# Performance work log

Hardware: AMD Instinct MI355X
Metric: run time of the kernel (lower is better)

Reference implementation:

```python
import jax, jax.numpy as jnp
import numpy as np

BN_EPS = 1e-5
DIST_EPS = 1e-8


def setup_inputs() -> dict:
    key = jax.random.key(0)
    ks = jax.random.split(key, 8)
    B, N, S, D1, D2 = 8, 16384, 2048, 128, 256
    return {
        "xyz1": jax.random.normal(ks[0], (B, N, 3), jnp.float32),
        "xyz2": jax.random.normal(ks[1], (B, S, 3), jnp.float32),
        "points1": jax.random.normal(ks[2], (B, N, D1), jnp.float32),
        "points2": jax.random.normal(ks[3], (B, S, D2), jnp.float32),
        "w1": jax.random.normal(ks[4], (256, 384), jnp.float32) * 0.05,
        "b1": jnp.zeros((256,), jnp.float32),
        "g1": jnp.ones((256,), jnp.float32),
        "be1": jnp.zeros((256,), jnp.float32),
        "w2": jax.random.normal(ks[5], (128, 256), jnp.float32) * 0.05,
        "b2": jnp.zeros((128,), jnp.float32),
        "g2": jnp.ones((128,), jnp.float32),
        "be2": jnp.zeros((128,), jnp.float32),
        "fa1": jax.random.normal(ks[6], (16, 128), jnp.float32) * 0.1,
        "fa2": jax.random.normal(ks[7], (128, 16), jnp.float32) * 0.1,
    }


def _three_interp(xyz1, xyz2, points2):
    # squared pairwise distance [B,N,S]
    d = (jnp.sum(xyz1 ** 2, -1)[:, :, None]
         + jnp.sum(xyz2 ** 2, -1)[:, None, :]
         - 2.0 * jnp.einsum("bnc,bsc->bns", xyz1, xyz2))
    neg_d, idx = jax.lax.top_k(-d, 3)          # 3 smallest distances
    dist = -neg_d                               # [B,N,3]
    recip = 1.0 / (dist + DIST_EPS)
    w = recip / jnp.sum(recip, -1, keepdims=True)
    B, N, _ = idx.shape
    D = points2.shape[-1]
    gathered = jnp.take_along_axis(
        points2, idx.reshape(B, N * 3)[..., None], axis=1
    ).reshape(B, N, 3, D)
    return jnp.sum(gathered * w[..., None], axis=-2)  # [B,N,D]


def _bn_relu(h, g, be):
    # train-mode BatchNorm1d: stats over (batch, length)
    mu = jnp.mean(h, axis=(0, 1))
    var = jnp.var(h, axis=(0, 1))
    return jax.nn.relu(g * (h - mu) / jnp.sqrt(var + BN_EPS) + be)


def reference(xyz1, xyz2, points1, points2, w1, b1, g1, be1,
              w2, b2, g2, be2, fa1, fa2):
    interp = _three_interp(xyz1, xyz2, points2)          # [B,N,256]
    x = jnp.concatenate([points1, interp], axis=-1)      # [B,N,384]
    # 1x1 Conv1d + BN + ReLU stack (channel-last)
    x = _bn_relu(jnp.einsum("bnc,oc->bno", x, w1) + b1, g1, be1)  # [B,N,256]
    x = _bn_relu(jnp.einsum("bnc,oc->bno", x, w2) + b2, g2, be2)  # [B,N,128]
    # channel attention (SE-style, avg + max pool over length)
    def fc(v):  # v: [B,C]
        return jax.nn.relu(v @ fa1.T) @ fa2.T
    avg = jnp.mean(x, axis=1)
    mx = jnp.max(x, axis=1)
    scale = jax.nn.sigmoid(fc(avg) + fc(mx))             # [B,C]
    return x * scale[:, None, :]                          # [B,N,128]
```

## Files before the change

### kernel.cpp

```cpp
#include <hip/hip_runtime.h>
#include <math.h>

constexpr int BB = 8;
constexpr int NN = 16384;
constexpr int SS = 2048;
constexpr int D2 = 256;
constexpr int H1 = 256;
constexpr int H2 = 128;
constexpr int MM = BB * NN;
constexpr int LDB = 40;

typedef __attribute__((ext_vector_type(8))) short short8;
typedef __attribute__((ext_vector_type(16))) float f32x16;

__device__ __forceinline__ unsigned short f2b(float f) {
    union { float f; unsigned u; } v; v.f = f;
    unsigned r = v.u + 0x7FFFu + ((v.u >> 16) & 1u);
    return (unsigned short)(r >> 16);
}
__device__ __forceinline__ unsigned pk2(float lo, float hi) {
    return (unsigned)f2b(lo) | ((unsigned)f2b(hi) << 16);
}
__device__ __forceinline__ float b2f_lo(unsigned p) { return __uint_as_float(p << 16); }
__device__ __forceinline__ float b2f_hi(unsigned p) { return __uint_as_float(p & 0xFFFF0000u); }

__global__ void k_init(float* __restrict__ st1, float* __restrict__ st2,
                       float* __restrict__ psum, int* __restrict__ pmax) {
    int t = threadIdx.x;
    if (t < 512) st1[t] = 0.f;
    if (t < 256) st2[t] = 0.f;
    if (t < 1024) { psum[t] = 0.f; pmax[t] = 0; }
}

__global__ void k_wprep(const float* __restrict__ w1, const float* __restrict__ w2,
                        unsigned short* __restrict__ w1b, unsigned short* __restrict__ w2b) {
    int i = blockIdx.x * 256 + threadIdx.x;
    if (i < H1 * 384) w1b[i] = f2b(w1[i]);
    if (i < H2 * 256) w2b[i] = f2b(w2[i]);
}

__global__ __launch_bounds__(256) void k_knn(const float* __restrict__ xyz1,
                                             const float* __restrict__ xyz2,
                                             int* __restrict__ idx,
                                             float* __restrict__ wgt) {
    __shared__ float sx[SS], sy[SS], sz[SS];
    __shared__ unsigned cand[64][20];
    const int b = blockIdx.y;
    const int tid = threadIdx.x;
    const int ql = tid & 63;
    const int chunk = tid >> 6;
    const int n = blockIdx.x * 64 + ql;

    const float* xz2 = xyz2 + (size_t)b * SS * 3;
    for (int s = tid; s < SS; s += 256) {
        sx[s] = xz2[s * 3 + 0];
        sy[s] = xz2[s * 3 + 1];
        sz[s] = xz2[s * 3 + 2];
    }
    __syncthreads();

    const float* q = xyz1 + ((size_t)b * NN + n) * 3;
    const float qx = q[0], qy = q[1], qz = q[2];

    unsigned k0 = 0xFFFFFFFFu, k1 = 0xFFFFFFFFu, k2 = 0xFFFFFFFFu,
             k3 = 0xFFFFFFFFu, k4 = 0xFFFFFFFFu;
    const int s0 = chunk * 512;
#pragma unroll 4
    for (int j = 0; j < 512; ++j) {
        const int s = s0 + j;
        const float dx = qx - sx[s];
        const float dy = qy - sy[s];
        const float dz = qz - sz[s];
        const float d = fmaf(dx, dx, fmaf(dy, dy, dz * dz));
        const unsigned key = (__float_as_uint(d) & 0xFFFFFE00u) | (unsigned)j;
        const bool c0 = key < k0, c1 = key < k1, c2 = key < k2,
                   c3 = key < k3, c4 = key < k4;
        k4 = c4 ? (c3 ? k3 : key) : k4;
        k3 = c3 ? (c2 ? k2 : key) : k3;
        k2 = c2 ? (c1 ? k1 : key) : k2;
        k1 = c1 ? (c0 ? k0 : key) : k1;
        k0 = c0 ? key : k0;
    }
    unsigned* cq = cand[ql] + chunk * 5;
    cq[0] = k0; cq[1] = k1; cq[2] = k2; cq[3] = k3; cq[4] = k4;
    __syncthreads();

    if (tid < 64) {
        const double qxd = (double)qx, qyd = (double)qy, qzd = (double)qz;
        double t0 = 1e300, t1 = 1e300, t2 = 1e300;
        int i0 = 0, i1 = 0, i2 = 0;
#pragma unroll
        for (int ch = 0; ch < 4; ++ch) {
#pragma unroll
            for (int t = 0; t < 5; ++t) {
                const int s = ch * 512 + (int)(cand[tid][ch * 5 + t] & 0x1FFu);
                const double dx = qxd - (double)sx[s];
                const double dy = qyd - (double)sy[s];
                const double dz = qzd - (double)sz[s];
                const double d = fma(dx, dx, fma(dy, dy, dz * dz));
                if (d < t2) {
                    if (d < t0)      { t2 = t1; i2 = i1; t1 = t0; i1 = i0; t0 = d; i0 = s; }
                    else if (d < t1) { t2 = t1; i2 = i1; t1 = d; i1 = s; }
                    else             { t2 = d; i2 = s; }
                }
            }
        }
        const double r0 = 1.0 / (t0 + 1e-8);
        const double r1 = 1.0 / (t1 + 1e-8);
        const double r2 = 1.0 / (t2 + 1e-8);
        const double inv = 1.0 / (r0 + r1 + r2);
        const size_t o = ((size_t)b * NN + n) * 3;
        idx[o + 0] = i0; idx[o + 1] = i1; idx[o + 2] = i2;
        wgt[o + 0] = (float)(r0 * inv);
        wgt[o + 1] = (float)(r1 * inv);
        wgt[o + 2] = (float)(r2 * inv);
    }
}

__global__ __launch_bounds__(256, 2) void k_gemm1(const float* __restrict__ p1,
                                                  const float* __restrict__ p2,
                                                  const int* __restrict__ idx,
                                                  const float* __restrict__ wgt,
                                                  const unsigned short* __restrict__ w1b,
                                                  const float* __restrict__ b1p,
                                                  unsigned short* __restrict__ h1b,
                                                  float* __restrict__ st1) {
    __shared__ __align__(16) unsigned short As[128 * LDB];
    __shared__ __align__(16) unsigned short Bs[256 * LDB];
    __shared__ float sSum[256], sSq[256];

    const int tid = threadIdx.x;
    const int row0 = blockIdx.x * 128;
    const int b = row0 >> 14;
    const float* p2b = p2 + (size_t)b * (SS * D2);

    sSum[tid] = 0.f; sSq[tid] = 0.f;

    const int wave = tid >> 6, lane = tid & 63;
    const int ln = lane & 31, hk = lane >> 5;
    const int wm = (wave & 1) << 6;
    const int wn = (wave >> 1) << 7;
    const int r = tid >> 1, half = tid & 1;

    const size_t o3 = (size_t)(row0 + r) * 3;
    const int j0 = idx[o3], j1 = idx[o3 + 1], j2 = idx[o3 + 2];
    const float wa = wgt[o3], wb = wgt[o3 + 1], wc = wgt[o3 + 2];
    const float* g0 = p2b + ((size_t)j0 << 8);
    const float* g1 = p2b + ((size_t)j1 << 8);
    const float* g2 = p2b + ((size_t)j2 << 8);

    f32x16 acc[2][4];
#pragma unroll
    for (int mt = 0; mt < 2; ++mt)
#pragma unroll
        for (int nt = 0; nt < 4; ++nt)
#pragma unroll
            for (int e = 0; e < 16; ++e) acc[mt][nt][e] = 0.f;

    float4 ra[12];
    uint4 rb[4];

    auto prefetch = [&](int kc) {
        const unsigned short* bsrc = w1b + (size_t)tid * 384 + kc * 32;
        rb[0] = *(const uint4*)(bsrc);
        rb[1] = *(const uint4*)(bsrc + 8);
        rb[2] = *(const uint4*)(bsrc + 16);
        rb[3] = *(const uint4*)(bsrc + 24);
        if (kc < 4) {
            const float* src = p1 + (((size_t)(row0 + r)) << 7) + kc * 32 + half * 16;
            ra[0] = *(const float4*)(src);
            ra[1] = *(const float4*)(src + 4);
            ra[2] = *(const float4*)(src + 8);
            ra[3] = *(const float4*)(src + 12);
        } else {
            const int c2 = kc * 32 - 128 + half * 16;
#pragma unroll
            for (int g = 0; g < 4; ++g) {
                ra[g]     = *(const float4*)(g0 + c2 + g * 4);
                ra[4 + g] = *(const float4*)(g1 + c2 + g * 4);
                ra[8 + g] = *(const float4*)(g2 + c2 + g * 4);
            }
        }
    };

    prefetch(0);

    for (int kc = 0; kc < 12; ++kc) {
        uint4 pa0, pa1;
        if (kc < 4) {
            pa0 = make_uint4(pk2(ra[0].x, ra[0].y), pk2(ra[0].z, ra[0].w),
                             pk2(ra[1].x, ra[1].y), pk2(ra[1].z, ra[1].w));
            pa1 = make_uint4(pk2(ra[2].x, ra[2].y), pk2(ra[2].z, ra[2].w),
                             pk2(ra[3].x, ra[3].y), pk2(ra[3].z, ra[3].w));
        } else {
            float v[16];
#pragma unroll
            for (int g = 0; g < 4; ++g) {
                v[g * 4 + 0] = fmaf(wa, ra[g].x, fmaf(wb, ra[4 + g].x, wc * ra[8 + g].x));
                v[g * 4 + 1] = fmaf(wa, ra[g].y, fmaf(wb, ra[4 + g].y, wc * ra[8 + g].y));
                v[g * 4 + 2] = fmaf(wa, ra[g].z, fmaf(wb, ra[4 + g].z, wc * ra[8 + g].z));
                v[g * 4 + 3] = fmaf(wa, ra[g].w, fmaf(wb, ra[4 + g].w, wc * ra[8 + g].w));
            }
            pa0 = make_uint4(pk2(v[0], v[1]), pk2(v[2], v[3]), pk2(v[4], v[5]), pk2(v[6], v[7]));
            pa1 = make_uint4(pk2(v[8], v[9]), pk2(v[10], v[11]), pk2(v[12], v[13]), pk2(v[14], v[15]));
        }
        const uint4 wb0 = rb[0], wb1 = rb[1], wb2 = rb[2], wb3 = rb[3];

        __syncthreads();
        *(uint4*)&As[r * LDB + half * 16] = pa0;
        *(uint4*)&As[r * LDB + half * 16 + 8] = pa1;
        *(uint4*)&Bs[tid * LDB + 0]  = wb0;
        *(uint4*)&Bs[tid * LDB + 8]  = wb1;
        *(uint4*)&Bs[tid * LDB + 16] = wb2;
        *(uint4*)&Bs[tid * LDB + 24] = wb3;
        __syncthreads();

        if (kc < 11) prefetch(kc + 1);

        short8 af[2][2], bfv[4][2];
#pragma unroll
        for (int mt = 0; mt < 2; ++mt)
#pragma unroll
            for (int ks = 0; ks < 2; ++ks)
                af[mt][ks] = *(const short8*)&As[(wm + mt * 32 + ln) * LDB + ks * 16 + hk * 8];
#pragma unroll
        for (int nt = 0; nt < 4; ++nt)
#pragma unroll
            for (int ks = 0; ks < 2; ++ks)
                bfv[nt][ks] = *(const short8*)&Bs[(wn + nt * 32 + ln) * LDB + ks * 16 + hk * 8];
#pragma unroll
        for (int mt = 0; mt < 2; ++mt)
#pragma unroll
            for (int nt = 0; nt < 4; ++nt)
#pragma unroll
                for (int ks = 0; ks < 2; ++ks)
                    acc[mt][nt] = __builtin_amdgcn_mfma_f32_32x32x16_bf16(
                        af[mt][ks], bfv[nt][ks], acc[mt][nt], 0, 0, 0);
    }

#pragma unroll
    for (int nt = 0; nt < 4; ++nt) {
        const int col = wn + nt * 32 + ln;
        const float bias = b1p[col];
        float ps = 0.f, pq = 0.f;
#pragma unroll
        for (int mt = 0; mt < 2; ++mt) {
#pragma unroll
            for (int e = 0; e < 16; ++e) {
                const int rl = wm + mt * 32 + (e & 3) + ((e >> 2) << 3) + (hk << 2);
                const float o = acc[mt][nt][e] + bias;
                ps += o;
                pq = fmaf(o, o, pq);
                h1b[(((size_t)(row0 + rl)) << 8) + col] = f2b(o);
            }
        }
        atomicAdd(&sSum[col], ps);
        atomicAdd(&sSq[col], pq);
    }
    __syncthreads();
    atomicAdd(&st1[tid], sSum[tid]);
    atomicAdd(&st1[256 + tid], sSq[tid]);
}

__global__ void k_bnprep(const float* __restrict__ st, const float* __restrict__ g,
                         const float* __restrict__ be, float* __restrict__ bn,
                         int C, float invM) {
    int c = blockIdx.x * blockDim.x + threadIdx.x;
    if (c < C) {
        float mean = st[c] * invM;
        float var = st[C + c] * invM - mean * mean;
        float a = g[c] / sqrtf(var + 1e-5f);
        bn[c] = a;
        bn[C + c] = fmaf(-mean, a, be[c]);
    }
}

__global__ __launch_bounds__(256) void k_gemm2(const unsigned short* __restrict__ h1b,
                                               const unsigned short* __restrict__ w2b,
                                               const float* __restrict__ b2p,
                                               const float* __restrict__ bn1,
                                               unsigned short* __restrict__ h2b,
                                               float* __restrict__ st2) {
    __shared__ __align__(16) unsigned short As[128 * LDB];
    __shared__ __align__(16) unsigned short Bs[128 * LDB];
    __shared__ float sBNa[256], sBNb[256];
    __shared__ float sSum[128], sSq[128];

    const int tid = threadIdx.x;
    const int row0 = blockIdx.x * 128;

    sBNa[tid] = bn1[tid];
    sBNb[tid] = bn1[256 + tid];
    if (tid < 128) { sSum[tid] = 0.f; sSq[tid] = 0.f; }

    const int wave = tid >> 6, lane = tid & 63;
    const int ln = lane & 31, hk = lane >> 5;
    const int wm = (wave & 1) << 6, wn = (wave >> 1) << 6;
    const int r = tid >> 1, half = tid & 1;

    f32x16 acc[2][2];
#pragma unroll
    for (int mt = 0; mt < 2; ++mt)
#pragma unroll
        for (int nt = 0; nt < 2; ++nt)
#pragma unroll
            for (int e = 0; e < 16; ++e) acc[mt][nt][e] = 0.f;

    uint4 rA0, rA1, rB0, rB1;
    auto prefetch = [&](int kc) {
        const unsigned short* asrc = h1b + (size_t)(row0 + r) * 256 + kc * 32 + half * 16;
        rA0 = *(const uint4*)asrc;
        rA1 = *(const uint4*)(asrc + 8);
        const unsigned short* bsrc = w2b + (size_t)r * 256 + kc * 32 + half * 16;
        rB0 = *(const uint4*)bsrc;
        rB1 = *(const uint4*)(bsrc + 8);
    };

    prefetch(0);
    __syncthreads();

    for (int kc = 0; kc < 8; ++kc) {
        const int k0 = kc * 32 + half * 16;
        unsigned pw[8] = {rA0.x, rA0.y, rA0.z, rA0.w, rA1.x, rA1.y, rA1.z, rA1.w};
        unsigned po[8];
#pragma unroll
        for (int gi = 0; gi < 8; ++gi) {
            float lo = b2f_lo(pw[gi]);
            float hi = b2f_hi(pw[gi]);
            lo = fmaxf(fmaf(sBNa[k0 + 2 * gi], lo, sBNb[k0 + 2 * gi]), 0.f);
            hi = fmaxf(fmaf(sBNa[k0 + 2 * gi + 1], hi, sBNb[k0 + 2 * gi + 1]), 0.f);
            po[gi] = pk2(lo, hi);
        }
        const uint4 pa0 = make_uint4(po[0], po[1], po[2], po[3]);
        const uint4 pa1 = make_uint4(po[4], po[5], po[6], po[7]);
        const uint4 qb0 = rB0, qb1 = rB1;

        __syncthreads();
        *(uint4*)&As[r * LDB + half * 16] = pa0;
        *(uint4*)&As[r * LDB + half * 16 + 8] = pa1;
        *(uint4*)&Bs[r * LDB + half * 16] = qb0;
        *(uint4*)&Bs[r * LDB + half * 16 + 8] = qb1;
        __syncthreads();

        if (kc < 7) prefetch(kc + 1);

        short8 af[2][2], bfv[2][2];
#pragma unroll
        for (int mt = 0; mt < 2; ++mt)
#pragma unroll
            for (int ks = 0; ks < 2; ++ks)
                af[mt][ks] = *(const short8*)&As[(wm + mt * 32 + ln) * LDB + ks * 16 + hk * 8];
#pragma unroll
        for (int nt = 0; nt < 2; ++nt)
#pragma unroll
            for (int ks = 0; ks < 2; ++ks)
                bfv[nt][ks] = *(const short8*)&Bs[(wn + nt * 32 + ln) * LDB + ks * 16 + hk * 8];
#pragma unroll
        for (int mt = 0; mt < 2; ++mt)
#pragma unroll
            for (int nt = 0; nt < 2; ++nt)
#pragma unroll
                for (int ks = 0; ks < 2; ++ks)
                    acc[mt][nt] = __builtin_amdgcn_mfma_f32_32x32x16_bf16(
                        af[mt][ks], bfv[nt][ks], acc[mt][nt], 0, 0, 0);
    }

#pragma unroll
    for (int nt = 0; nt < 2; ++nt) {
        const int col = wn + nt * 32 + ln;
        const float bias = b2p[col];
        float ps = 0.f, pq = 0.f;
#pragma unroll
        for (int mt = 0; mt < 2; ++mt) {
#pragma unroll
            for (int e = 0; e < 16; ++e) {
                const int rl = wm + mt * 32 + (e & 3) + ((e >> 2) << 3) + (hk << 2);
                const float o = acc[mt][nt][e] + bias;
                ps += o;
                pq = fmaf(o, o, pq);
                h2b[(((size_t)(row0 + rl)) << 7) + col] = f2b(o);
            }
        }
        atomicAdd(&sSum[col], ps);
        atomicAdd(&sSq[col], pq);
    }
    __syncthreads();
    if (tid < 128) {
        atomicAdd(&st2[tid], sSum[tid]);
        atomicAdd(&st2[128 + tid], sSq[tid]);
    }
}

__global__ __launch_bounds__(256) void k_pool(const unsigned short* __restrict__ h2b,
                                              const float* __restrict__ bn2,
                                              float* __restrict__ psum,
                                              int* __restrict__ pmax) {
    const int b = blockIdx.y;
    const int n0 = blockIdx.x * 256;
    const int tid = threadIdx.x;
    const int c = tid & 127, rh = tid >> 7;
    const float a = bn2[c], bc = bn2[128 + c];
    const unsigned short* base = h2b + (((size_t)b * NN + n0 + rh) << 7) + c;
    float s = 0.f, m = 0.f;
    for (int i = 0; i < 128; ++i) {
        float v = __uint_as_float((unsigned)base[(size_t)i * 256] << 16);
        float x = fmaxf(fmaf(a, v, bc), 0.f);
        s += x;
        m = fmaxf(m, x);
    }
    __shared__ float rs[256];
    __shared__ float rm[256];
    rs[tid] = s; rm[tid] = m;
    __syncthreads();
    if (tid < 128) {
        float ts = rs[tid] + rs[tid + 128];
        float tm = fmaxf(rm[tid], rm[tid + 128]);
        atomicAdd(&psum[b * 128 + c], ts);
        atomicMax(&pmax[b * 128 + c], __float_as_int(tm));
    }
}

__global__ __launch_bounds__(1024) void k_attn(const float* __restrict__ psum,
                                               const int* __restrict__ pmax,
                                               const float* __restrict__ fa1,
                                               const float* __restrict__ fa2,
                                               const float* __restrict__ bn2,
                                               float* __restrict__ sa,
                                               float* __restrict__ sb) {
    __shared__ float tS[128];
    const int tid = threadIdx.x;
    if (tid < 128) {
        const int b = tid >> 4, j = tid & 15;
        float da = 0.f, dm = 0.f;
        for (int cc = 0; cc < 128; ++cc) {
            float f = fa1[j * 128 + cc];
            da = fmaf(psum[b * 128 + cc] * (1.0f / 16384.0f), f, da);
            dm = fmaf(__int_as_float(pmax[b * 128 + cc]), f, dm);
        }
        tS[tid] = fmaxf(da, 0.f) + fmaxf(dm, 0.f);
    }
    __syncthreads();
    const int b = tid >> 7, c = tid & 127;
    float s = 0.f;
#pragma unroll
    for (int j = 0; j < 16; ++j) s = fmaf(tS[b * 16 + j], fa2[c * 16 + j], s);
    const float sc = 1.f / (1.f + expf(-s));
    sa[b * 128 + c] = bn2[c] * sc;
    sb[b * 128 + c] = bn2[128 + c] * sc;
}

__global__ void k_final(const unsigned short* __restrict__ h2b, const float* __restrict__ sa,
                        const float* __restrict__ sb, float* __restrict__ out) {
    const size_t i = (size_t)blockIdx.x * blockDim.x + threadIdx.x;
    const int cg = (int)(i & 15) * 8;
    const size_t row = i >> 4;
    const int b = (int)(row >> 14);
    const uint4 h = *(const uint4*)(h2b + (row << 7) + cg);
    const float4 A0 = *(const float4*)&sa[b * 128 + cg];
    const float4 A1 = *(const float4*)&sa[b * 128 + cg + 4];
    const float4 B0 = *(const float4*)&sb[b * 128 + cg];
    const float4 B1 = *(const float4*)&sb[b * 128 + cg + 4];
    float4 o0, o1;
    o0.x = fmaxf(fmaf(A0.x, b2f_lo(h.x), B0.x), 0.f);
    o0.y = fmaxf(fmaf(A0.y, b2f_hi(h.x), B0.y), 0.f);
    o0.z = fmaxf(fmaf(A0.z, b2f_lo(h.y), B0.z), 0.f);
    o0.w = fmaxf(fmaf(A0.w, b2f_hi(h.y), B0.w), 0.f);
    o1.x = fmaxf(fmaf(A1.x, b2f_lo(h.z), B1.x), 0.f);
    o1.y = fmaxf(fmaf(A1.y, b2f_hi(h.z), B1.y), 0.f);
    o1.z = fmaxf(fmaf(A1.z, b2f_lo(h.w), B1.z), 0.f);
    o1.w = fmaxf(fmaf(A1.w, b2f_hi(h.w), B1.w), 0.f);
    *(float4*)(out + (row << 7) + cg) = o0;
    *(float4*)(out + (row << 7) + cg + 4) = o1;
}

extern "C" void kernel_launch(void* const* d_in, const int* in_sizes, int n_in,
                              void* d_out, int out_size, void* d_ws, size_t ws_size,
                              hipStream_t stream) {
    const float* xyz1 = (const float*)d_in[0];
    const float* xyz2 = (const float*)d_in[1];
    const float* p1   = (const float*)d_in[2];
    const float* p2   = (const float*)d_in[3];
    const float* w1   = (const float*)d_in[4];
    const float* b1   = (const float*)d_in[5];
    const float* g1   = (const float*)d_in[6];
    const float* be1  = (const float*)d_in[7];
    const float* w2   = (const float*)d_in[8];
    const float* b2   = (const float*)d_in[9];
    const float* g2   = (const float*)d_in[10];
    const float* be2  = (const float*)d_in[11];
    const float* fa1  = (const float*)d_in[12];
    const float* fa2  = (const float*)d_in[13];
    float* out = (float*)d_out;

    char* ws = (char*)d_ws;
    int*   idx  = (int*)ws;
    float* wgt  = (float*)(ws + 1572864);
    unsigned short* h1b = (unsigned short*)(ws + 3145728);
    unsigned short* h2b = (unsigned short*)(ws + 70254592);
    float* st1  = (float*)(ws + 103809024);
    float* bn1  = st1 + 512;
    float* st2  = bn1 + 512;
    float* bn2  = st2 + 256;
    float* psum = bn2 + 256;
    int*   pmax = (int*)(psum + 1024);
    float* sa   = (float*)(pmax + 1024);
    float* sb   = sa + 1024;
    unsigned short* w1b = (unsigned short*)(sb + 1024);
    unsigned short* w2b = w1b + 98304;

    k_init<<<1, 1024, 0, stream>>>(st1, st2, psum, pmax);
    k_wprep<<<(H1 * 384 + 255) / 256, 256, 0, stream>>>(w1, w2, w1b, w2b);
    k_knn<<<dim3(NN / 64, BB), 256, 0, stream>>>(xyz1, xyz2, idx, wgt);
    k_gemm1<<<MM / 128, 256, 0, stream>>>(p1, p2, idx, wgt, w1b, b1, h1b, st1);
    k_bnprep<<<1, 256, 0, stream>>>(st1, g1, be1, bn1, 256, 1.0f / (float)MM);
    k_gemm2<<<MM / 128, 256, 0, stream>>>(h1b, w2b, b2, bn1, h2b, st2);
    k_bnprep<<<1, 128, 0, stream>>>(st2, g2, be2, bn2, 128, 1.0f / (float)MM);
    k_pool<<<dim3(NN / 256, BB), 256, 0, stream>>>(h2b, bn2, psum, pmax);
    k_attn<<<1, 1024, 0, stream>>>(psum, pmax, fa1, fa2, bn2, sa, sb);
    k_final<<<(MM * H2 / 8) / 256, 256, 0, stream>>>(h2b, sa, sb, out);
}
```

Measured before the change: 447.6 us.

## Stream padded xyz2 via scalar loads in KNN and shrink candidate list

Adds a prep kernel that packs xyz2 into float4 records, and has the KNN kernel read them directly from global memory. The chunk index is made wave-uniform so these reads can be scalar/broadcast loads, replacing the LDS staging and the block sync. Each thread keeps four candidates per chunk instead of five, updated with a min/max insertion network rather than nested selects. The refinement pass gathers its candidates from global memory, and the smaller candidate list slightly narrows the safety margin of the quantised-key prefilter.

```diff
diff --git a/kernel.cpp b/kernel.cpp
--- a/kernel.cpp
+++ b/kernel.cpp
@@ -39,50 +39,46 @@
     if (i < H2 * 256) w2b[i] = f2b(w2[i]);
 }
 
+__global__ void k_xyzprep(const float* __restrict__ xyz2, float4* __restrict__ xyz2p) {
+    int i = blockIdx.x * 256 + threadIdx.x;
+    if (i < BB * SS) {
+        xyz2p[i] = make_float4(xyz2[i * 3], xyz2[i * 3 + 1], xyz2[i * 3 + 2], 0.f);
+    }
+}
+
 __global__ __launch_bounds__(256) void k_knn(const float* __restrict__ xyz1,
-                                             const float* __restrict__ xyz2,
+                                             const float4* __restrict__ xyz2p,
                                              int* __restrict__ idx,
                                              float* __restrict__ wgt) {
-    __shared__ float sx[SS], sy[SS], sz[SS];
-    __shared__ unsigned cand[64][20];
+    __shared__ unsigned cand[64][16];
     const int b = blockIdx.y;
     const int tid = threadIdx.x;
     const int ql = tid & 63;
-    const int chunk = tid >> 6;
     const int n = blockIdx.x * 64 + ql;
-
-    const float* xz2 = xyz2 + (size_t)b * SS * 3;
-    for (int s = tid; s < SS; s += 256) {
-        sx[s] = xz2[s * 3 + 0];
-        sy[s] = xz2[s * 3 + 1];
-        sz[s] = xz2[s * 3 + 2];
-    }
-    __syncthreads();
 
     const float* q = xyz1 + ((size_t)b * NN + n) * 3;
     const float qx = q[0], qy = q[1], qz = q[2];
 
-    unsigned k0 = 0xFFFFFFFFu, k1 = 0xFFFFFFFFu, k2 = 0xFFFFFFFFu,
-             k3 = 0xFFFFFFFFu, k4 = 0xFFFFFFFFu;
-    const int s0 = chunk * 512;
+    const int chunk = __builtin_amdgcn_readfirstlane(tid >> 6);
+    const float4* cp = xyz2p + ((size_t)b << 11) + (chunk << 9);
+
+    unsigned k0 = 0xFFFFFFFFu, k1 = 0xFFFFFFFFu, k2 = 0xFFFFFFFFu, k3 = 0xFFFFFFFFu;
 #pragma unroll 4
     for (int j = 0; j < 512; ++j) {
-        const int s = s0 + j;
-        const float dx = qx - sx[s];
-        const float dy = qy - sy[s];
-        const float dz = qz - sz[s];
+        const float4 p = cp[j];
+        const float dx = qx - p.x;
+        const float dy = qy - p.y;
+        const float dz = qz - p.z;
         const float d = fmaf(dx, dx, fmaf(dy, dy, dz * dz));
         const unsigned key = (__float_as_uint(d) & 0xFFFFFE00u) | (unsigned)j;
-        const bool c0 = key < k0, c1 = key < k1, c2 = key < k2,
-                   c3 = key < k3, c4 = key < k4;
-        k4 = c4 ? (c3 ? k3 : key) : k4;
-        k3 = c3 ? (c2 ? k2 : key) : k3;
-        k2 = c2 ? (c1 ? k1 : key) : k2;
-        k1 = c1 ? (c0 ? k0 : key) : k1;
-        k0 = c0 ? key : k0;
-    }
-    unsigned* cq = cand[ql] + chunk * 5;
-    cq[0] = k0; cq[1] = k1; cq[2] = k2; cq[3] = k3; cq[4] = k4;
+        unsigned m;
+        m  = max(k0, key); k0 = min(k0, key);
+        unsigned m2 = max(k1, m); k1 = min(k1, m);
+        unsigned m3 = max(k2, m2); k2 = min(k2, m2);
+        k3 = min(k3, m3);
+    }
+    unsigned* cq = cand[ql] + chunk * 4;
+    cq[0] = k0; cq[1] = k1; cq[2] = k2; cq[3] = k3;
     __syncthreads();
 
     if (tid < 64) {
@@ -90,19 +86,17 @@
         double t0 = 1e300, t1 = 1e300, t2 = 1e300;
         int i0 = 0, i1 = 0, i2 = 0;
 #pragma unroll
-        for (int ch = 0; ch < 4; ++ch) {
-#pragma unroll
-            for (int t = 0; t < 5; ++t) {
-                const int s = ch * 512 + (int)(cand[tid][ch * 5 + t] & 0x1FFu);
-                const double dx = qxd - (double)sx[s];
-                const double dy = qyd - (double)sy[s];
-                const double dz = qzd - (double)sz[s];
-                const double d = fma(dx, dx, fma(dy, dy, dz * dz));
-                if (d < t2) {
-                    if (d < t0)      { t2 = t1; i2 = i1; t1 = t0; i1 = i0; t0 = d; i0 = s; }
-                    else if (d < t1) { t2 = t1; i2 = i1; t1 = d; i1 = s; }
-                    else             { t2 = d; i2 = s; }
-                }
+        for (int c = 0; c < 16; ++c) {
+            const int s = ((c >> 2) << 9) + (int)(cand[tid][c] & 0x1FFu);
+            const float4 p = xyz2p[((size_t)b << 11) + s];
+            const double dx = qxd - (double)p.x;
+            const double dy = qyd - (double)p.y;
+            const double dz = qzd - (double)p.z;
+            const double d = fma(dx, dx, fma(dy, dy, dz * dz));
+            if (d < t2) {
+                if (d < t0)      { t2 = t1; i2 = i1; t1 = t0; i1 = i0; t0 = d; i0 = s; }
+                else if (d < t1) { t2 = t1; i2 = i1; t1 = d; i1 = s; }
+                else             { t2 = d; i2 = s; }
             }
         }
         const double r0 = 1.0 / (t0 + 1e-8);
@@ -507,10 +501,12 @@
     float* sb   = sa + 1024;
     unsigned short* w1b = (unsigned short*)(sb + 1024);
     unsigned short* w2b = w1b + 98304;
+    float4* xyz2p = (float4*)(ws + 104857600);
 
     k_init<<<1, 1024, 0, stream>>>(st1, st2, psum, pmax);
     k_wprep<<<(H1 * 384 + 255) / 256, 256, 0, stream>>>(w1, w2, w1b, w2b);
-    k_knn<<<dim3(NN / 64, BB), 256, 0, stream>>>(xyz1, xyz2, idx, wgt);
+    k_xyzprep<<<(BB * SS + 255) / 256, 256, 0, stream>>>(xyz2, xyz2p);
+    k_knn<<<dim3(NN / 64, BB), 256, 0, stream>>>(xyz1, xyz2p, idx, wgt);
     k_gemm1<<<MM / 128, 256, 0, stream>>>(p1, p2, idx, wgt, w1b, b1, h1b, st1);
     k_bnprep<<<1, 256, 0, stream>>>(st1, g1, be1, bn1, 256, 1.0f / (float)MM);
     k_gemm2<<<MM / 128, 256, 0, stream>>>(h1b, w2b, b2, bn1, h2b, st2);
```

Measured after the change: 417.3 us. 1.07x faster.
